# Kernel tuning notes

Hardware: AMD Instinct MI355X
Metric: run time of the kernel (lower is better)

Reference implementation:

```python
import jax, jax.numpy as jnp
import numpy as np

N, n, d = 4, 2048, 1024


def setup_inputs() -> dict:
    key = jax.random.key(0)
    k1, k2, k3, k4 = jax.random.split(key, 4)
    x = jax.random.normal(k1, (N, n, d), dtype=jnp.float32)
    mask = jax.random.randint(k2, (N, n, n), 0, 2, dtype=jnp.int32)
    Wqk = jax.random.normal(k3, (d, d), dtype=jnp.float32) * (d ** -0.5)
    Wvc = jax.random.normal(k4, (d, d), dtype=jnp.float32) * (d ** -0.5)
    return {"x": x, "mask": mask, "Wqk": Wqk, "Wvc": Wvc}


def reference(x, mask, Wqk, Wvc):
    # q = Wqk(x): torch Linear computes x @ W^T
    q = jnp.einsum('bnd,ed->bne', x, Wqk)          # [N, n, d]
    scale = jnp.asarray(x.shape[-1], x.dtype) ** 0.5
    scores = jnp.einsum('bnd,bmd->bnm', q, x) / scale  # [N, n, n]
    scores = jnp.where(mask == 0, jnp.asarray(-1e20, scores.dtype), scores)
    attention = jax.nn.softmax(scores, axis=-1)
    attended = jnp.einsum('bnm,bmd->bnd', attention, x)
    return jnp.einsum('bnd,ed->bne', attended, Wvc)
```

## Files before the change

kernel.cpp:

```cpp
#include <hip/hip_runtime.h>
#include <hip/hip_bf16.h>

typedef short bf16x8 __attribute__((ext_vector_type(8)));
typedef short s16x4  __attribute__((ext_vector_type(4)));
typedef short s16x8  __attribute__((ext_vector_type(8)));
typedef float f32x4  __attribute__((ext_vector_type(4)));

static __device__ __forceinline__ void async_cp16(const void* g, void* l) {
  __builtin_amdgcn_global_load_lds(
      (const __attribute__((address_space(1))) unsigned int*)g,
      (__attribute__((address_space(3))) unsigned int*)l, 16, 0, 0);
}

static __device__ __forceinline__ unsigned short f2bf_bits(float f) {
  union { __hip_bfloat16 b; unsigned short u; } cv;
  cv.b = __float2bfloat16(f);
  return cv.u;
}
static __device__ __forceinline__ float bf2f(short u) {
  union { float f; unsigned v; } cv;
  cv.v = ((unsigned)(unsigned short)u) << 16;
  return cv.f;
}

#define BAR() __builtin_amdgcn_s_barrier()
#define SBZ() __builtin_amdgcn_sched_barrier(0)
#define LGKM0() do { asm volatile("s_waitcnt lgkmcnt(0)" ::: "memory"); SBZ(); } while (0)
#define VMW(n) do { asm volatile("s_waitcnt vmcnt(" #n ")" ::: "memory"); SBZ(); } while (0)

__global__ __launch_bounds__(256) void cvt_all(const float* __restrict__ x,
                                               const float* __restrict__ wqk,
                                               const float* __restrict__ wvc,
                                               __hip_bfloat16* __restrict__ xb,
                                               __hip_bfloat16* __restrict__ wqkb,
                                               __hip_bfloat16* __restrict__ wvcb) {
  const int b = blockIdx.x;
  const float* in;
  __hip_bfloat16* out;
  long base;
  if (b < 8192)       { in = x;   out = xb;   base = (long)b * 1024; }
  else if (b < 9216)  { in = wqk; out = wqkb; base = (long)(b - 8192) * 1024; }
  else                { in = wvc; out = wvcb; base = (long)(b - 9216) * 1024; }
  const long i = base + threadIdx.x * 4;
  const float4 v = *(const float4*)(in + i);
  s16x4 o;
  o[0] = (short)f2bf_bits(v.x);
  o[1] = (short)f2bf_bits(v.y);
  o[2] = (short)f2bf_bits(v.z);
  o[3] = (short)f2bf_bits(v.w);
  *(s16x4*)(out + i) = o;
}

struct GemmDesc {
  const __hip_bfloat16* A; const __hip_bfloat16* B; void* C;
  int lda, ldb, ldc, nT, tpb; long sA, sB, sC; float cscale;
};

template<int MODE>
__global__ __launch_bounds__(512, 2) void gemm8p(GemmDesc g0, GemmDesc g1, int nb0, int K) {
  __shared__ char lds[131072];
  const int bid = blockIdx.x, nwg = gridDim.x;
  const int wg = (bid & 7) * (nwg >> 3) + (bid >> 3);
  GemmDesc g = (wg < nb0) ? g0 : g1;
  const int id = (wg < nb0) ? wg : wg - nb0;
  const int bz = id / g.tpb, tl = id - bz * g.tpb;
  const int bm = tl / g.nT, bn = tl - bm * g.nT;
  const long m0 = (long)bm * 256, n0 = (long)bn * 256;
  const __hip_bfloat16* Ab = g.A + bz * g.sA;
  const __hip_bfloat16* Bb = g.B + bz * g.sB;

  const int t = threadIdx.x, lane = t & 63, w = t >> 6;
  const int wm = w >> 2, wn = w & 3;
  const int lr = lane & 15, cs = lane >> 4;

  const int srow = t >> 3;
  const int sslot = (t & 7) ^ (srow & 7);
  const __hip_bfloat16* aP[2][2];
  const __hip_bfloat16* bP[2][2];
  #pragma unroll
  for (int h = 0; h < 2; ++h)
    #pragma unroll
    for (int i = 0; i < 2; ++i) {
      aP[h][i] = Ab + (m0 + h * 128 + i * 64 + srow) * g.lda + sslot * 8;
      bP[h][i] = Bb + (n0 + h * 128 + i * 64 + srow) * g.ldb + sslot * 8;
    }

  int aOf[8], bOf[4];
  #pragma unroll
  for (int mm = 0; mm < 8; ++mm)
    aOf[mm] = wm * 16384 + (mm * 16 + lr) * 128 + ((cs ^ (lr & 7)) << 4);
  #pragma unroll
  for (int nf = 0; nf < 4; ++nf)
    bOf[nf] = 32768 + (wn >> 1) * 16384 + ((wn & 1) * 64 + nf * 16 + lr) * 128 +
              ((cs ^ (lr & 7)) << 4);

  f32x4 acc[8][4] = {};
  bf16x8 af[4][2], bqA[2][2], bqB[2][2];

  #define STG(P, h, kt, dbase) do { \
    async_cp16(P[h][0] + (long)(kt) * 64, lds + (dbase) + t * 16); \
    async_cp16(P[h][1] + (long)(kt) * 64, lds + (dbase) + 8192 + t * 16); } while (0)
  #define RD_AF(mb, bufb) do { _Pragma("unroll") for (int mm_ = 0; mm_ < 4; ++mm_) { \
      af[mm_][0] = *(const bf16x8*)(lds + (bufb) + aOf[(mb) * 4 + mm_]); \
      af[mm_][1] = *(const bf16x8*)(lds + (bufb) + (aOf[(mb) * 4 + mm_] ^ 64)); } } while (0)
  #define RD_BQ(dst, nb, bufb) do { _Pragma("unroll") for (int nf_ = 0; nf_ < 2; ++nf_) { \
      dst[nf_][0] = *(const bf16x8*)(lds + (bufb) + bOf[(nb) * 2 + nf_]); \
      dst[nf_][1] = *(const bf16x8*)(lds + (bufb) + (bOf[(nb) * 2 + nf_] ^ 64)); } } while (0)
  #define MM16(BQ, NB, MB) do { \
    __builtin_amdgcn_s_setprio(1); \
    _Pragma("unroll") for (int ks_ = 0; ks_ < 2; ++ks_) \
      _Pragma("unroll") for (int mm_ = 0; mm_ < 4; ++mm_) \
        _Pragma("unroll") for (int nf_ = 0; nf_ < 2; ++nf_) \
          acc[(MB) + mm_][(NB) + nf_] = __builtin_amdgcn_mfma_f32_16x16x32_bf16( \
              af[mm_][ks_], BQ[nf_][ks_], acc[(MB) + mm_][(NB) + nf_], 0, 0, 0); \
    __builtin_amdgcn_s_setprio(0); } while (0)

  const int nt = K >> 6, nJ = nt >> 1;
  STG(bP, 0, 0, 32768); STG(bP, 1, 0, 49152);
  STG(aP, 0, 0, 0);     STG(aP, 1, 0, 16384);
  STG(bP, 0, 1, 65536 + 32768); STG(bP, 1, 1, 65536 + 49152);
  VMW(4);
  BAR(); SBZ();

  for (int j = 0; j < nJ; ++j) {
    const bool full = (j + 1 < nJ);
    const int tb = 2 * j + 1, ta2 = 2 * j + 2, tb2 = 2 * j + 3;
    RD_AF(0, 0); RD_BQ(bqA, 0, 0);
    STG(aP, 0, tb, 65536);
    LGKM0();
    MM16(bqA, 0, 0);
    BAR(); SBZ();
    RD_BQ(bqB, 1, 0);
    STG(aP, 1, tb, 65536 + 16384);
    LGKM0();
    MM16(bqB, 2, 0);
    BAR(); SBZ();
    RD_AF(1, 0);
    if (full) STG(bP, 0, ta2, 32768);
    LGKM0();
    MM16(bqB, 2, 4);
    BAR(); SBZ();
    if (full) STG(bP, 1, ta2, 49152);
    MM16(bqA, 0, 4);
    if (full) { VMW(4); } else { VMW(0); }
    BAR(); SBZ();
    RD_AF(0, 65536); RD_BQ(bqA, 0, 65536);
    if (full) STG(aP, 0, ta2, 0);
    LGKM0();
    MM16(bqA, 0, 0);
    BAR(); SBZ();
    RD_BQ(bqB, 1, 65536);
    if (full) STG(aP, 1, ta2, 16384);
    LGKM0();
    MM16(bqB, 2, 0);
    BAR(); SBZ();
    RD_AF(1, 65536);
    if (full) STG(bP, 0, tb2, 65536 + 32768);
    LGKM0();
    MM16(bqB, 2, 4);
    BAR(); SBZ();
    if (full) STG(bP, 1, tb2, 65536 + 49152);
    MM16(bqA, 0, 4);
    if (full) { VMW(4); } else { VMW(0); }
    BAR(); SBZ();
  }
  #undef STG
  #undef RD_AF
  #undef RD_BQ
  #undef MM16

  const long crow0 = m0 + wm * 128 + cs * 4;
  const long ccol0 = n0 + wn * 64 + lr;
  if (MODE == 0) {
    float* C = (float*)g.C + bz * g.sC;
    #pragma unroll
    for (int mm = 0; mm < 8; ++mm)
      #pragma unroll
      for (int nf = 0; nf < 4; ++nf)
        #pragma unroll
        for (int rr = 0; rr < 4; ++rr)
          C[(crow0 + mm * 16 + rr) * g.ldc + ccol0 + nf * 16] = acc[mm][nf][rr];
  } else {
    __hip_bfloat16* C = (__hip_bfloat16*)g.C + bz * g.sC;
    #pragma unroll
    for (int mm = 0; mm < 8; ++mm)
      #pragma unroll
      for (int nf = 0; nf < 4; ++nf)
        #pragma unroll
        for (int rr = 0; rr < 4; ++rr)
          C[(crow0 + mm * 16 + rr) * g.ldc + ccol0 + nf * 16] =
              __float2bfloat16(acc[mm][nf][rr] * g.cscale);
  }
}

template<int MODE, int WM, int WN, int MR_, int MINW>
__global__ __launch_bounds__(512, MINW) void gemm8w(GemmDesc g0, GemmDesc g1, int nb0, int K) {
  constexpr int BM    = WM * MR_ * 16;
  constexpr int BN    = WN * 64;
  constexpr int BOFF  = BM * 64;
  constexpr int BUFSZ = (BM + BN) * 64;
  constexpr int KW    = (BM + BN) / 128;
  __shared__ char lds[3 * BUFSZ];

  const int bid = blockIdx.x, nwg = gridDim.x;
  const int wg = (bid & 7) * (nwg >> 3) + (bid >> 3);
  GemmDesc g = (wg < nb0) ? g0 : g1;
  const int id = (wg < nb0) ? wg : wg - nb0;
  const int bz = id / g.tpb, tl = id - bz * g.tpb;
  const int bm = tl / g.nT, bn = tl - bm * g.nT;
  const long m0 = (long)bm * BM, n0 = (long)bn * BN;
  const __hip_bfloat16* Ab = g.A + bz * g.sA;
  const __hip_bfloat16* Bb = g.B + bz * g.sB;

  const int t = threadIdx.x;
  const int lane = t & 63, w = t >> 6;
  const int wm = w / WN, wn = w % WN;
  const int lr = lane & 15, cs = lane >> 4;

  const int rA  = t >> 2;
  const int dsl = t & 3;
  const int ssl = dsl ^ ((rA >> 1) & 3);
  const __hip_bfloat16* aSt0 = Ab + (m0 + rA) * g.lda + ssl * 8;
  const __hip_bfloat16* aSt1 = Ab + (m0 + 128 + rA) * g.lda + ssl * 8;
  const __hip_bfloat16* bSt0 = Bb + (n0 + rA) * g.ldb + ssl * 8;
  const __hip_bfloat16* bSt1 = Bb + (n0 + 128 + rA) * g.ldb + ssl * 8;

  const int axor = ((lr >> 1) & 3) << 4;
  int aRd[MR_], bRd[4];
  #pragma unroll
  for (int mm = 0; mm < MR_; ++mm)
    aRd[mm] = (wm * (MR_ * 16) + mm * 16 + lr) * 64 + ((cs << 4) ^ axor);
  #pragma unroll
  for (int nf = 0; nf < 4; ++nf)
    bRd[nf] = BOFF + (wn * 64 + nf * 16 + lr) * 64 + ((cs << 4) ^ axor);

  f32x4 acc[MR_][4] = {};

  #define STAGE(kt, base) do { \
    async_cp16(aSt0 + (long)(kt) * 32, lds + (base) + t * 16); \
    if constexpr (BM == 256) \
      async_cp16(aSt1 + (long)(kt) * 32, lds + (base) + 8192 + t * 16); \
    async_cp16(bSt0 + (long)(kt) * 32, lds + (base) + BOFF + t * 16); \
    if constexpr (BN == 256) \
      async_cp16(bSt1 + (long)(kt) * 32, lds + (base) + BOFF + 8192 + t * 16); \
  } while (0)
  #define VM_KW() do { if constexpr (KW == 4) { VMW(4); } else { VMW(3); } } while (0)

  const int nt = K >> 5;
  STAGE(0, 0);
  STAGE(1, BUFSZ);
  VM_KW();
  BAR();

  int rb = 0, sb = 2 * BUFSZ;
  for (int tt = 0; tt < nt; ++tt) {
    bf16x8 af[MR_], bq[4];
    #pragma unroll
    for (int mm = 0; mm < MR_; ++mm)
      af[mm] = *(const bf16x8*)(lds + rb + aRd[mm]);
    #pragma unroll
    for (int nf = 0; nf < 4; ++nf)
      bq[nf] = *(const bf16x8*)(lds + rb + bRd[nf]);
    if (tt + 2 < nt) STAGE(tt + 2, sb);
    #pragma unroll
    for (int mm = 0; mm < MR_; ++mm)
      #pragma unroll
      for (int nf = 0; nf < 4; ++nf)
        acc[mm][nf] = __builtin_amdgcn_mfma_f32_16x16x32_bf16(af[mm], bq[nf], acc[mm][nf], 0, 0, 0);
    if (tt + 2 < nt) { VM_KW(); } else { VMW(0); }
    BAR();
    rb = (rb == 2 * BUFSZ) ? 0 : rb + BUFSZ;
    sb = (sb == 2 * BUFSZ) ? 0 : sb + BUFSZ;
  }
  #undef STAGE
  #undef VM_KW

  const long crow0 = m0 + wm * (MR_ * 16) + cs * 4;
  const long ccol0 = n0 + wn * 64 + lr;
  if (MODE == 0) {
    float* C = (float*)g.C + bz * g.sC;
    #pragma unroll
    for (int mm = 0; mm < MR_; ++mm)
      #pragma unroll
      for (int nf = 0; nf < 4; ++nf)
        #pragma unroll
        for (int rr = 0; rr < 4; ++rr)
          C[(crow0 + mm * 16 + rr) * g.ldc + ccol0 + nf * 16] = acc[mm][nf][rr];
  } else {
    __hip_bfloat16* C = (__hip_bfloat16*)g.C + bz * g.sC;
    #pragma unroll
    for (int mm = 0; mm < MR_; ++mm)
      #pragma unroll
      for (int nf = 0; nf < 4; ++nf)
        #pragma unroll
        for (int rr = 0; rr < 4; ++rr)
          C[(crow0 + mm * 16 + rr) * g.ldc + ccol0 + nf * 16] =
              __float2bfloat16(acc[mm][nf][rr] * g.cscale);
  }
}

__global__ __launch_bounds__(256) void softmax_rows(__hip_bfloat16* __restrict__ S,
                                                    const int* __restrict__ Mask) {
  const long row = blockIdx.x;
  short* srow = (short*)(S + row * 2048);
  const int* mrow = Mask + row * 2048;
  const int t = threadIdx.x;
  const s16x8 sv = *(const s16x8*)(srow + t * 8);
  const int4 q0 = *(const int4*)(mrow + t * 8);
  const int4 q1 = *(const int4*)(mrow + t * 8 + 4);
  const int mk[8] = {q0.x, q0.y, q0.z, q0.w, q1.x, q1.y, q1.z, q1.w};

  float e[8];
  float s = 0.f;
  #pragma unroll
  for (int i = 0; i < 8; ++i) {
    e[i] = mk[i] ? __expf(bf2f(sv[i])) : 0.f;
    s += e[i];
  }
  #pragma unroll
  for (int off = 32; off > 0; off >>= 1) s += __shfl_xor(s, off);
  __shared__ float reds[4];
  if ((t & 63) == 0) reds[t >> 6] = s;
  __syncthreads();
  s = reds[0] + reds[1] + reds[2] + reds[3];

  s16x8 o;
  if (s > 0.f) {
    const float inv = 1.f / s;
    #pragma unroll
    for (int i = 0; i < 8; ++i) o[i] = (short)f2bf_bits(e[i] * inv);
  } else {
    const unsigned short u = f2bf_bits(1.f / 2048.f);
    #pragma unroll
    for (int i = 0; i < 8; ++i) o[i] = (short)u;
  }
  *(s16x8*)(srow + t * 8) = o;
}

extern "C" void kernel_launch(void* const* d_in, const int* in_sizes, int n_in,
                              void* d_out, int out_size, void* d_ws, size_t ws_size,
                              hipStream_t stream) {
  const float* x   = (const float*)d_in[0];
  const int*   msk = (const int*)d_in[1];
  const float* Wqk = (const float*)d_in[2];
  const float* Wvc = (const float*)d_in[3];
  float* out = (float*)d_out;
  char* ws = (char*)d_ws;

  __hip_bfloat16* xb   = (__hip_bfloat16*)(ws + 0);
  __hip_bfloat16* qb   = (__hip_bfloat16*)(ws + 16777216);
  __hip_bfloat16* vT   = (__hip_bfloat16*)(ws + 33554432);
  __hip_bfloat16* wqkb = (__hip_bfloat16*)(ws + 50331648);
  __hip_bfloat16* wvcb = (__hip_bfloat16*)(ws + 52428800);
  __hip_bfloat16* Sbf  = (__hip_bfloat16*)(ws + 54525952);

  cvt_all<<<dim3(10240), 256, 0, stream>>>(x, Wqk, Wvc, xb, wqkb, wvcb);

  GemmDesc gq{xb,   wqkb, qb, 1024, 1024, 1024, 4, 128, 0L, 0L, 0L, 0.03125f};
  GemmDesc gv{wvcb, xb,   vT, 1024, 1024, 2048, 8, 32, 0L, 2097152L, 2097152L, 1.f};
  gemm8p<1><<<dim3(256), 512, 0, stream>>>(gq, gv, 128, 1024);

  GemmDesc gs{qb, xb, Sbf, 1024, 1024, 2048, 8, 64, 2097152L, 2097152L, 4194304L, 1.f};
  gemm8p<1><<<dim3(256), 512, 0, stream>>>(gs, gs, 256, 1024);

  softmax_rows<<<dim3(8192), 256, 0, stream>>>(Sbf, msk);

  GemmDesc go{Sbf, vT, out, 2048, 2048, 1024, 8, 64, 4194304L, 2097152L, 2097152L, 1.f};
  gemm8w<0, 4, 2, 4, 4><<<dim3(256), 512, 0, stream>>>(go, go, 256, 2048);
}
```

Baseline: 141.5 us.

## Replace final attention-output GEMM with 16-wave kernel using a 64-deep K step

The last GEMM (softmax probabilities times V) moves from the 8-wave 256x128 tile kernel to a new 16-wave (1024-thread) kernel. It uses a 128x256 tile and loads 64 K-elements per stage, with a 128-byte-row LDS swizzle. The goal is more waves per block for latency hiding and half as many barrier and pipeline iterations along K. In exchange the triple-buffered LDS footprint grows to about 144 KB, which limits residency to one block per CU, and register pressure rises from holding two K-slices of fragments.

```diff
diff --git a/kernel.cpp b/kernel.cpp
--- a/kernel.cpp
+++ b/kernel.cpp
@@ -193,13 +193,14 @@
   }
 }
 
-template<int MODE, int WM, int WN, int MR_, int MINW>
-__global__ __launch_bounds__(512, MINW) void gemm8w(GemmDesc g0, GemmDesc g1, int nb0, int K) {
-  constexpr int BM    = WM * MR_ * 16;
-  constexpr int BN    = WN * 64;
-  constexpr int BOFF  = BM * 64;
-  constexpr int BUFSZ = (BM + BN) * 64;
-  constexpr int KW    = (BM + BN) / 128;
+template<int MODE, int BM_, int BK_>
+__global__ __launch_bounds__(1024, 4) void gemm16(GemmDesc g0, GemmDesc g1, int nb0, int K) {
+  constexpr int MR = BM_ / 64;
+  constexpr int KR = BK_ / 32;
+  constexpr int W  = BK_ * 2;
+  constexpr int NB = (256 * W) / 16384;
+  constexpr int BUFSZ = 16384 + NB * 16384;
+  constexpr int KW = 1 + NB;
   __shared__ char lds[3 * BUFSZ];
 
   const int bid = blockIdx.x, nwg = gridDim.x;
@@ -208,45 +209,45 @@
   const int id = (wg < nb0) ? wg : wg - nb0;
   const int bz = id / g.tpb, tl = id - bz * g.tpb;
   const int bm = tl / g.nT, bn = tl - bm * g.nT;
-  const long m0 = (long)bm * BM, n0 = (long)bn * BN;
+  const long m0 = (long)bm * BM_, n0 = (long)bn * 256;
   const __hip_bfloat16* Ab = g.A + bz * g.sA;
   const __hip_bfloat16* Bb = g.B + bz * g.sB;
 
   const int t = threadIdx.x;
   const int lane = t & 63, w = t >> 6;
-  const int wm = w / WN, wn = w % WN;
+  const int wm = w >> 2, wn = w & 3;
   const int lr = lane & 15, cs = lane >> 4;
 
-  const int rA  = t >> 2;
-  const int dsl = t & 3;
-  const int ssl = dsl ^ ((rA >> 1) & 3);
-  const __hip_bfloat16* aSt0 = Ab + (m0 + rA) * g.lda + ssl * 8;
-  const __hip_bfloat16* aSt1 = Ab + (m0 + 128 + rA) * g.lda + ssl * 8;
+  const int rA  = t / (W / 16);
+  const int dsl = t % (W / 16);
+  const int ssl = dsl ^ ((W == 64) ? ((rA >> 1) & 3) : (rA & 7));
+  const __hip_bfloat16* aSt  = Ab + (m0 + rA) * g.lda + ssl * 8;
   const __hip_bfloat16* bSt0 = Bb + (n0 + rA) * g.ldb + ssl * 8;
   const __hip_bfloat16* bSt1 = Bb + (n0 + 128 + rA) * g.ldb + ssl * 8;
 
-  const int axor = ((lr >> 1) & 3) << 4;
-  int aRd[MR_], bRd[4];
-  #pragma unroll
-  for (int mm = 0; mm < MR_; ++mm)
-    aRd[mm] = (wm * (MR_ * 16) + mm * 16 + lr) * 64 + ((cs << 4) ^ axor);
+  const int axor = (W == 64) ? (((lr >> 1) & 3) << 4) : ((lr & 7) << 4);
+  int aRd[MR][KR], bRd[4][KR];
+  #pragma unroll
+  for (int mm = 0; mm < MR; ++mm)
+    #pragma unroll
+    for (int ks = 0; ks < KR; ++ks)
+      aRd[mm][ks] = (wm * (BM_ / 4) + mm * 16 + lr) * W + ((((ks * 4 + cs) << 4) ^ axor));
   #pragma unroll
   for (int nf = 0; nf < 4; ++nf)
-    bRd[nf] = BOFF + (wn * 64 + nf * 16 + lr) * 64 + ((cs << 4) ^ axor);
-
-  f32x4 acc[MR_][4] = {};
+    #pragma unroll
+    for (int ks = 0; ks < KR; ++ks)
+      bRd[nf][ks] = 16384 + (wn * 64 + nf * 16 + lr) * W + ((((ks * 4 + cs) << 4) ^ axor));
+
+  f32x4 acc[MR][4] = {};
 
   #define STAGE(kt, base) do { \
-    async_cp16(aSt0 + (long)(kt) * 32, lds + (base) + t * 16); \
-    if constexpr (BM == 256) \
-      async_cp16(aSt1 + (long)(kt) * 32, lds + (base) + 8192 + t * 16); \
-    async_cp16(bSt0 + (long)(kt) * 32, lds + (base) + BOFF + t * 16); \
-    if constexpr (BN == 256) \
-      async_cp16(bSt1 + (long)(kt) * 32, lds + (base) + BOFF + 8192 + t * 16); \
+    async_cp16(aSt + (long)(kt) * BK_, lds + (base) + t * 16); \
+    async_cp16(bSt0 + (long)(kt) * BK_, lds + (base) + 16384 + t * 16); \
+    if (NB == 2) async_cp16(bSt1 + (long)(kt) * BK_, lds + (base) + 32768 + t * 16); \
   } while (0)
-  #define VM_KW() do { if constexpr (KW == 4) { VMW(4); } else { VMW(3); } } while (0)
-
-  const int nt = K >> 5;
+  #define VM_KW() do { if constexpr (KW == 2) { VMW(2); } else { VMW(3); } } while (0)
+
+  const int nt = K / BK_;
   STAGE(0, 0);
   STAGE(1, BUFSZ);
   VM_KW();
@@ -254,19 +255,25 @@
 
   int rb = 0, sb = 2 * BUFSZ;
   for (int tt = 0; tt < nt; ++tt) {
-    bf16x8 af[MR_], bq[4];
-    #pragma unroll
-    for (int mm = 0; mm < MR_; ++mm)
-      af[mm] = *(const bf16x8*)(lds + rb + aRd[mm]);
+    bf16x8 af[MR][KR], bq[4][KR];
+    #pragma unroll
+    for (int mm = 0; mm < MR; ++mm)
+      #pragma unroll
+      for (int ks = 0; ks < KR; ++ks)
+        af[mm][ks] = *(const bf16x8*)(lds + rb + aRd[mm][ks]);
     #pragma unroll
     for (int nf = 0; nf < 4; ++nf)
-      bq[nf] = *(const bf16x8*)(lds + rb + bRd[nf]);
+      #pragma unroll
+      for (int ks = 0; ks < KR; ++ks)
+        bq[nf][ks] = *(const bf16x8*)(lds + rb + bRd[nf][ks]);
     if (tt + 2 < nt) STAGE(tt + 2, sb);
     #pragma unroll
-    for (int mm = 0; mm < MR_; ++mm)
-      #pragma unroll
-      for (int nf = 0; nf < 4; ++nf)
-        acc[mm][nf] = __builtin_amdgcn_mfma_f32_16x16x32_bf16(af[mm], bq[nf], acc[mm][nf], 0, 0, 0);
+    for (int ks = 0; ks < KR; ++ks)
+      #pragma unroll
+      for (int mm = 0; mm < MR; ++mm)
+        #pragma unroll
+        for (int nf = 0; nf < 4; ++nf)
+          acc[mm][nf] = __builtin_amdgcn_mfma_f32_16x16x32_bf16(af[mm][ks], bq[nf][ks], acc[mm][nf], 0, 0, 0);
     if (tt + 2 < nt) { VM_KW(); } else { VMW(0); }
     BAR();
     rb = (rb == 2 * BUFSZ) ? 0 : rb + BUFSZ;
@@ -275,12 +282,12 @@
   #undef STAGE
   #undef VM_KW
 
-  const long crow0 = m0 + wm * (MR_ * 16) + cs * 4;
+  const long crow0 = m0 + wm * (BM_ / 4) + cs * 4;
   const long ccol0 = n0 + wn * 64 + lr;
   if (MODE == 0) {
     float* C = (float*)g.C + bz * g.sC;
     #pragma unroll
-    for (int mm = 0; mm < MR_; ++mm)
+    for (int mm = 0; mm < MR; ++mm)
       #pragma unroll
       for (int nf = 0; nf < 4; ++nf)
         #pragma unroll
@@ -289,7 +296,7 @@
   } else {
     __hip_bfloat16* C = (__hip_bfloat16*)g.C + bz * g.sC;
     #pragma unroll
-    for (int mm = 0; mm < MR_; ++mm)
+    for (int mm = 0; mm < MR; ++mm)
       #pragma unroll
       for (int nf = 0; nf < 4; ++nf)
         #pragma unroll
@@ -365,6 +372,6 @@
 
   softmax_rows<<<dim3(8192), 256, 0, stream>>>(Sbf, msk);
 
-  GemmDesc go{Sbf, vT, out, 2048, 2048, 1024, 8, 64, 4194304L, 2097152L, 2097152L, 1.f};
-  gemm8w<0, 4, 2, 4, 4><<<dim3(256), 512, 0, stream>>>(go, go, 256, 2048);
-}
+  GemmDesc go{Sbf, vT, out, 2048, 2048, 1024, 4, 64, 4194304L, 2097152L, 2097152L, 1.f};
+  gemm16<0, 128, 64><<<dim3(256), 1024, 0, stream>>>(go, go, 256, 2048);
+}
```

Result: no change. 139.0 us (median of 3 runs) (-1.8%).
